# Kernel optimization log

Measured on AMD Instinct MI355X. Metric: run time of the kernel, lower is better.

The kernel has to match this reference:

```python
import jax, jax.numpy as jnp
import numpy as np

GRAY = 0.2989 + 0.5870 + 0.1140  # tf.image.rgb_to_grayscale weight sum (channels identical after grayscale_to_rgb)


def _resample(img, coords, axis):
    """Bilinear 1-D resample of `img` along `axis` at float `coords` (clamped)."""
    n = img.shape[axis]
    i0f = jnp.floor(coords)
    i0 = jnp.clip(i0f, 0, n - 1).astype(jnp.int32)
    i1 = jnp.clip(i0f + 1.0, 0, n - 1).astype(jnp.int32)
    f = coords - i0f
    a = jnp.take(img, i0, axis=axis)
    b = jnp.take(img, i1, axis=axis)
    shp = [1] * img.ndim
    shp[axis] = -1
    f = f.reshape(shp)
    return a * (1.0 - f) + b * f


def _aug_one(img, off_f, b, c, size, docrop, flp, k):
    S = img.shape[0]
    # ---- random crop (prob 0.5) + bilinear resize back to SxS (half-pixel centers) ----
    size_f = jnp.where(docrop, size.astype(jnp.float32), float(S))
    off = jnp.where(docrop, jnp.floor(off_f * (S - size_f + 1.0)), 0.0)  # [2] integer-valued offsets
    idx = (jnp.arange(S, dtype=jnp.float32) + 0.5) * (size_f / S) - 0.5
    img = _resample(img, idx + off[0], 0)
    img = _resample(img, idx + off[1], 1)
    # ---- random flip_left_right + rot90(k) ----
    img = jnp.where(flp, img[:, ::-1, :], img)
    rots = jnp.stack([img,
                      jnp.rot90(img, 1, (0, 1)),
                      jnp.rot90(img, 2, (0, 1)),
                      jnp.rot90(img, 3, (0, 1))])
    img = rots[k]
    # ---- per-channel brightness + contrast (gray->rgb->gray round trip == GRAY scale) ----
    x = img + b  # [S,S,C] + [C]
    m = jnp.mean(x, axis=(0, 1), keepdims=True)
    x = (x - m) * c + m
    return x * GRAY


def setup_inputs() -> dict:
    B, S, C = 64, 256, 5
    key = jax.random.key(0)
    ks = jax.random.split(key, 8)
    crops = jax.random.normal(ks[0], (B, S, S, C), dtype=jnp.float32)
    crop_size = jax.random.randint(ks[1], (B,), int(0.8 * S), S, dtype=jnp.int32)
    do_crop = jax.random.uniform(ks[2], (B,)) < 0.5
    off_frac = jax.random.uniform(ks[3], (B, 2), dtype=jnp.float32)
    flip = jax.random.uniform(ks[4], (B,)) < 0.5
    rot_k = jax.random.randint(ks[5], (B,), 0, 4, dtype=jnp.int32)
    bright = jax.random.uniform(ks[6], (B, C), minval=-0.1, maxval=0.1, dtype=jnp.float32)
    contrast = jax.random.uniform(ks[7], (B, C), minval=0.8, maxval=1.2, dtype=jnp.float32)
    return {"crops": crops, "off_frac": off_frac, "bright": bright, "contrast": contrast,
            "crop_size": crop_size, "do_crop": do_crop, "flip": flip, "rot_k": rot_k}


def reference(crops, off_frac, bright, contrast, crop_size, do_crop, flip, rot_k):
    return jax.vmap(_aug_one)(crops, off_frac, bright, contrast, crop_size, do_crop, flip, rot_k)
```

## Files before the change

### kernel.cpp

```cpp
#include <hip/hip_runtime.h>
#include <math.h>

#define SDIM 256
#define CH 5
#define ROWF (SDIM * CH)
#define NCHUNK 32
#define CHROWS 8
#define GRAYF 0.9999f

__global__ __launch_bounds__(256) void aug_sums_kernel(
    const float* __restrict__ crops,
    const float* __restrict__ off_frac,
    const int*   __restrict__ crop_size,
    const int*   __restrict__ do_crop,
    float* __restrict__ part)
{
    const int chunk = blockIdx.x;
    const int b     = blockIdx.y;
    const int tid   = threadIdx.x;

    __shared__ __align__(16) float wyl[SDIM];
    __shared__ __align__(16) float wxl[SDIM];
    __shared__ float psum[4][CH];

    const bool  docrop = do_crop[b] != 0;
    const float size_f = docrop ? (float)crop_size[b] : 256.0f;
    const float scale  = size_f * (1.0f / 256.0f);
    const float span   = 256.0f - size_f + 1.0f;
    const float off0   = docrop ? floorf(off_frac[2 * b + 0] * span) : 0.0f;
    const float off1   = docrop ? floorf(off_frac[2 * b + 1] * span) : 0.0f;

    wyl[tid] = 0.0f;
    wxl[tid] = 0.0f;
    __syncthreads();

    {
        const float cy = ((float)tid + 0.5f) * scale - 0.5f + off0;
        const float fl = floorf(cy);
        const float fy = cy - fl;
        const int r0 = min(max((int)fl, 0), 255);
        const int r1 = min(max((int)fl + 1, 0), 255);
        atomicAdd(&wyl[r0], 1.0f - fy);
        atomicAdd(&wyl[r1], fy);

        const float cx = ((float)tid + 0.5f) * scale - 0.5f + off1;
        const float fl2 = floorf(cx);
        const float fx  = cx - fl2;
        const int c0 = min(max((int)fl2, 0), 255);
        const int c1 = min(max((int)fl2 + 1, 0), 255);
        atomicAdd(&wxl[c0], 1.0f - fx);
        atomicAdd(&wxl[c1], fx);
    }
    __syncthreads();

    const float* srcbase = crops + ((size_t)b * SDIM + (size_t)chunk * CHROWS) * ROWF;
    const int rA = tid >> 6;
    const int rB = rA + 4;
    const int t  = tid & 63;

    const float4* pA = reinterpret_cast<const float4*>(srcbase + rA * ROWF + t * 20);
    const float4* pB = reinterpret_cast<const float4*>(srcbase + rB * ROWF + t * 20);
    const float4 a0 = pA[0], a1 = pA[1], a2 = pA[2], a3 = pA[3], a4 = pA[4];
    const float4 b0 = pB[0], b1 = pB[1], b2 = pB[2], b3 = pB[3], b4 = pB[4];

    const float wrA = wyl[chunk * CHROWS + rA];
    const float wrB = wyl[chunk * CHROWS + rB];
    const float4 wx = reinterpret_cast<const float4*>(wxl)[t];

    float acc[5] = {0.0f, 0.0f, 0.0f, 0.0f, 0.0f};
    {
        const float w0 = wx.x * wrA, w1 = wx.y * wrA, w2 = wx.z * wrA, w3 = wx.w * wrA;
        acc[0] += a0.x * w0; acc[1] += a0.y * w0; acc[2] += a0.z * w0; acc[3] += a0.w * w0;
        acc[4] += a1.x * w0; acc[0] += a1.y * w1; acc[1] += a1.z * w1; acc[2] += a1.w * w1;
        acc[3] += a2.x * w1; acc[4] += a2.y * w1; acc[0] += a2.z * w2; acc[1] += a2.w * w2;
        acc[2] += a3.x * w2; acc[3] += a3.y * w2; acc[4] += a3.z * w2; acc[0] += a3.w * w3;
        acc[1] += a4.x * w3; acc[2] += a4.y * w3; acc[3] += a4.z * w3; acc[4] += a4.w * w3;
    }
    {
        const float w0 = wx.x * wrB, w1 = wx.y * wrB, w2 = wx.z * wrB, w3 = wx.w * wrB;
        acc[0] += b0.x * w0; acc[1] += b0.y * w0; acc[2] += b0.z * w0; acc[3] += b0.w * w0;
        acc[4] += b1.x * w0; acc[0] += b1.y * w1; acc[1] += b1.z * w1; acc[2] += b1.w * w1;
        acc[3] += b2.x * w1; acc[4] += b2.y * w1; acc[0] += b2.z * w2; acc[1] += b2.w * w2;
        acc[2] += b3.x * w2; acc[3] += b3.y * w2; acc[4] += b3.z * w2; acc[0] += b3.w * w3;
        acc[1] += b4.x * w3; acc[2] += b4.y * w3; acc[3] += b4.z * w3; acc[4] += b4.w * w3;
    }

    const int lane = tid & 63;
    const int wv   = tid >> 6;
    #pragma unroll
    for (int ch = 0; ch < CH; ++ch) {
        float s = acc[ch];
        #pragma unroll
        for (int o = 32; o > 0; o >>= 1) s += __shfl_down(s, o, 64);
        if (lane == 0) psum[wv][ch] = s;
    }
    __syncthreads();
    if (tid == 0) {
        #pragma unroll
        for (int ch = 0; ch < CH; ++ch)
            part[((size_t)chunk * 64 + b) * CH + ch] =
                psum[0][ch] + psum[1][ch] + psum[2][ch] + psum[3][ch];
    }
}

__global__ __launch_bounds__(256) void aug_out_kernel(
    const float* __restrict__ crops,
    const float* __restrict__ off_frac,
    const int*   __restrict__ crop_size,
    const int*   __restrict__ do_crop,
    const int*   __restrict__ flip,
    const int*   __restrict__ rot_k,
    const float* __restrict__ part,
    const float* __restrict__ bright,
    const float* __restrict__ contrast,
    float* __restrict__ out)
{
    const int oi0  = blockIdx.x * 4;
    const int b    = blockIdx.y;
    const int tid  = threadIdx.x;
    const int rr   = tid >> 6;
    const int lane = tid & 63;

    __shared__ __align__(16) float smem[28 * 260];
    __shared__ float prm[2 * CH];

    const bool  docrop = do_crop[b] != 0;
    const float size_f = docrop ? (float)crop_size[b] : 256.0f;
    const float scale  = size_f * (1.0f / 256.0f);
    const float span   = 256.0f - size_f + 1.0f;
    const float off0   = docrop ? floorf(off_frac[2 * b + 0] * span) : 0.0f;
    const float off1   = docrop ? floorf(off_frac[2 * b + 1] * span) : 0.0f;
    const int   k      = rot_k[b] & 3;
    const bool  flp    = flip[b] != 0;

    if (tid < CH) {
        float s = 0.0f;
        #pragma unroll
        for (int p = 0; p < NCHUNK; ++p) s += part[((size_t)p * 64 + b) * CH + tid];
        const float m  = s * (1.0f / 65536.0f);
        const float co = contrast[b * CH + tid];
        const float br = bright[b * CH + tid];
        prm[tid]      = co * GRAYF;
        prm[CH + tid] = ((1.0f - co) * m + br) * GRAYF;
    }

    float vout[20];

    if ((k & 1) == 0) {
        const int y_min = (k == 0) ? oi0 : 255 - (oi0 + 3);
        const float cymin = ((float)y_min + 0.5f) * scale - 0.5f + off0;
        const int rbase = (int)floorf(cymin);
        const int nst   = docrop ? 5 : 4;

        const float4* src4 = reinterpret_cast<const float4*>(crops + (size_t)b * SDIM * ROWF);
        float4* dst4 = reinterpret_cast<float4*>(smem);
        for (int i = tid; i < nst * 320; i += 256) {
            const int w  = i / 320;
            const int f4 = i - w * 320;
            const int rc = min(max(rbase + w, 0), 255);
            dst4[i] = src4[rc * 320 + f4];
        }
        __syncthreads();

        const int oi = oi0 + rr;
        const int y  = (k == 0) ? oi : 255 - oi;

        if (!docrop) {
            const float* rb = smem + (y - rbase) * ROWF;
            #pragma unroll
            for (int p = 0; p < 4; ++p) {
                const int oj = lane + 64 * p;
                const int xf = (k == 0) ? oj : 255 - oj;
                const int x  = flp ? 255 - xf : xf;
                #pragma unroll
                for (int ch = 0; ch < CH; ++ch) vout[p * 5 + ch] = rb[x * CH + ch];
            }
        } else {
            const float cy  = ((float)y + 0.5f) * scale - 0.5f + off0;
            const float flr = floorf(cy);
            const float fy  = cy - flr;
            const float* rbA = smem + ((int)flr - rbase) * ROWF;
            const float* rbB = rbA + ROWF;
            #pragma unroll
            for (int p = 0; p < 4; ++p) {
                const int oj = lane + 64 * p;
                const int xf = (k == 0) ? oj : 255 - oj;
                const int x  = flp ? 255 - xf : xf;
                const float cx  = ((float)x + 0.5f) * scale - 0.5f + off1;
                const float fl2 = floorf(cx);
                const float fx  = cx - fl2;
                const int c0 = min(max((int)fl2, 0), 255);
                const int c1 = min(max((int)fl2 + 1, 0), 255);
                #pragma unroll
                for (int ch = 0; ch < CH; ++ch) {
                    const float aV = rbA[c0 * CH + ch] + fx * (rbA[c1 * CH + ch] - rbA[c0 * CH + ch]);
                    const float dV = rbB[c0 * CH + ch] + fx * (rbB[c1 * CH + ch] - rbB[c0 * CH + ch]);
                    vout[p * 5 + ch] = aV + fy * (dV - aV);
                }
            }
        }
    } else {
        const int xfA = (k == 1) ? 255 - oi0 : oi0;
        const int xfB = (k == 1) ? 255 - (oi0 + 3) : oi0 + 3;
        const int xA = flp ? 255 - xfA : xfA;
        const int xB = flp ? 255 - xfB : xfB;
        const int xmin = min(xA, xB);

        if (!docrop) {
            const int base4 = min((xmin * CH) & ~3, ROWF - 24);
            const float4* rp = reinterpret_cast<const float4*>(
                crops + ((size_t)b * SDIM + tid) * ROWF + base4);
            const float4 q0 = rp[0], q1 = rp[1], q2 = rp[2];
            const float4 q3 = rp[3], q4 = rp[4], q5 = rp[5];
            smem[ 0*260+tid]=q0.x; smem[ 1*260+tid]=q0.y; smem[ 2*260+tid]=q0.z; smem[ 3*260+tid]=q0.w;
            smem[ 4*260+tid]=q1.x; smem[ 5*260+tid]=q1.y; smem[ 6*260+tid]=q1.z; smem[ 7*260+tid]=q1.w;
            smem[ 8*260+tid]=q2.x; smem[ 9*260+tid]=q2.y; smem[10*260+tid]=q2.z; smem[11*260+tid]=q2.w;
            smem[12*260+tid]=q3.x; smem[13*260+tid]=q3.y; smem[14*260+tid]=q3.z; smem[15*260+tid]=q3.w;
            smem[16*260+tid]=q4.x; smem[17*260+tid]=q4.y; smem[18*260+tid]=q4.z; smem[19*260+tid]=q4.w;
            smem[20*260+tid]=q5.x; smem[21*260+tid]=q5.y; smem[22*260+tid]=q5.z; smem[23*260+tid]=q5.w;
            __syncthreads();

            const int oi = oi0 + rr;
            const int xf = (k == 1) ? 255 - oi : oi;
            const int x  = flp ? 255 - xf : xf;
            const int slotA = x * CH - base4;
            #pragma unroll
            for (int p = 0; p < 4; ++p) {
                const int oj = lane + 64 * p;
                const int y  = (k == 1) ? oj : 255 - oj;
                #pragma unroll
                for (int ch = 0; ch < CH; ++ch)
                    vout[p * 5 + ch] = smem[(slotA + ch) * 260 + y];
            }
        } else {
            const float cxmin = ((float)xmin + 0.5f) * scale - 0.5f + off1;
            const int cbase = (int)floorf(cxmin);
            const int base4 = (cbase * CH) & ~3;
            const bool fastp = (cbase >= 0) && (cbase + 4 <= 255) && (base4 >= 0) && (base4 + 28 <= ROWF);

            if (fastp) {
                const float4* rp = reinterpret_cast<const float4*>(
                    crops + ((size_t)b * SDIM + tid) * ROWF + base4);
                const float4 q0 = rp[0], q1 = rp[1], q2 = rp[2], q3 = rp[3];
                const float4 q4 = rp[4], q5 = rp[5], q6 = rp[6];
                smem[ 0*260+tid]=q0.x; smem[ 1*260+tid]=q0.y; smem[ 2*260+tid]=q0.z; smem[ 3*260+tid]=q0.w;
                smem[ 4*260+tid]=q1.x; smem[ 5*260+tid]=q1.y; smem[ 6*260+tid]=q1.z; smem[ 7*260+tid]=q1.w;
                smem[ 8*260+tid]=q2.x; smem[ 9*260+tid]=q2.y; smem[10*260+tid]=q2.z; smem[11*260+tid]=q2.w;
                smem[12*260+tid]=q3.x; smem[13*260+tid]=q3.y; smem[14*260+tid]=q3.z; smem[15*260+tid]=q3.w;
                smem[16*260+tid]=q4.x; smem[17*260+tid]=q4.y; smem[18*260+tid]=q4.z; smem[19*260+tid]=q4.w;
                smem[20*260+tid]=q5.x; smem[21*260+tid]=q5.y; smem[22*260+tid]=q5.z; smem[23*260+tid]=q5.w;
                smem[24*260+tid]=q6.x; smem[25*260+tid]=q6.y; smem[26*260+tid]=q6.z; smem[27*260+tid]=q6.w;
            } else {
                #pragma unroll
                for (int w = 0; w < 28; ++w) {
                    const int f2 = base4 + w + ROWF;
                    const int c2 = f2 / 5;
                    const int ch = f2 - c2 * 5;
                    const int cc = min(max(c2 - 256, 0), 255);
                    smem[w * 260 + tid] = crops[((size_t)b * SDIM + tid) * ROWF + cc * CH + ch];
                }
            }
            __syncthreads();

            const int oi = oi0 + rr;
            const int xf = (k == 1) ? 255 - oi : oi;
            const int x  = flp ? 255 - xf : xf;
            const float cx  = ((float)x + 0.5f) * scale - 0.5f + off1;
            const float fl2 = floorf(cx);
            const float fx  = cx - fl2;
            const int slotA = (int)fl2 * CH - base4;
            const int slotB = slotA + CH;

            #pragma unroll
            for (int p = 0; p < 4; ++p) {
                const int oj = lane + 64 * p;
                const int y  = (k == 1) ? oj : 255 - oj;
                const float cy  = ((float)y + 0.5f) * scale - 0.5f + off0;
                const float flr = floorf(cy);
                const float fy  = cy - flr;
                const int r0 = min(max((int)flr, 0), 255);
                const int r1 = min(max((int)flr + 1, 0), 255);
                #pragma unroll
                for (int ch = 0; ch < CH; ++ch) {
                    const float p00 = smem[(slotA + ch) * 260 + r0];
                    const float p01 = smem[(slotB + ch) * 260 + r0];
                    const float p10 = smem[(slotA + ch) * 260 + r1];
                    const float p11 = smem[(slotB + ch) * 260 + r1];
                    const float aV = p00 + fx * (p01 - p00);
                    const float dV = p10 + fx * (p11 - p10);
                    vout[p * 5 + ch] = aV + fy * (dV - aV);
                }
            }
        }
    }

    float aa[5], ab[5];
    #pragma unroll
    for (int ch = 0; ch < CH; ++ch) { aa[ch] = prm[ch]; ab[ch] = prm[CH + ch]; }
    #pragma unroll
    for (int p = 0; p < 4; ++p)
        #pragma unroll
        for (int ch = 0; ch < CH; ++ch)
            vout[p * 5 + ch] = vout[p * 5 + ch] * aa[ch] + ab[ch];

    __syncthreads();
    #pragma unroll
    for (int p = 0; p < 4; ++p) {
        const int oj = lane + 64 * p;
        #pragma unroll
        for (int ch = 0; ch < CH; ++ch)
            smem[rr * ROWF + oj * CH + ch] = vout[p * 5 + ch];
    }
    __syncthreads();

    const float4* ob4 = reinterpret_cast<const float4*>(smem);
    float4* dst = reinterpret_cast<float4*>(out + ((size_t)b * SDIM + oi0) * ROWF);
    #pragma unroll
    for (int q = 0; q < 5; ++q) dst[q * 256 + tid] = ob4[q * 256 + tid];
}

extern "C" void kernel_launch(void* const* d_in, const int* in_sizes, int n_in,
                              void* d_out, int out_size, void* d_ws, size_t ws_size,
                              hipStream_t stream) {
    const float* crops     = (const float*)d_in[0];
    const float* off_frac  = (const float*)d_in[1];
    const float* bright    = (const float*)d_in[2];
    const float* contrast  = (const float*)d_in[3];
    const int*   crop_size = (const int*)d_in[4];
    const int*   do_crop   = (const int*)d_in[5];
    const int*   flipb     = (const int*)d_in[6];
    const int*   rot_k     = (const int*)d_in[7];

    float* out  = (float*)d_out;
    float* part = (float*)d_ws;

    dim3 blk(256);
    aug_sums_kernel<<<dim3(NCHUNK, 64), blk, 0, stream>>>(crops, off_frac, crop_size, do_crop, part);
    aug_out_kernel<<<dim3(SDIM / 4, 64), blk, 0, stream>>>(crops, off_frac, crop_size, do_crop,
                                                           flipb, rot_k, part, bright, contrast, out);
}
```

Baseline: 184.3 us.

## Fuse mean-reduction and output kernels into one kernel with redundant per-block sums

Merges the partial-sum kernel and the output kernel into a single launch of 512 blocks, eight per image. Each block recomputes the full weighted channel mean for its image, then produces 32 output rows over 8 loop iterations. This removes the second launch and the workspace round trip for partial sums. In exchange, each image is read eight times for the reduction, and the grid is much smaller, which lowers parallelism and latency hiding.

```diff
diff --git a/kernel.cpp b/kernel.cpp
--- a/kernel.cpp
+++ b/kernel.cpp
@@ -4,24 +4,28 @@
 #define SDIM 256
 #define CH 5
 #define ROWF (SDIM * CH)
-#define NCHUNK 32
-#define CHROWS 8
 #define GRAYF 0.9999f
 
-__global__ __launch_bounds__(256) void aug_sums_kernel(
+__global__ __launch_bounds__(256) void aug_fused_kernel(
     const float* __restrict__ crops,
     const float* __restrict__ off_frac,
     const int*   __restrict__ crop_size,
     const int*   __restrict__ do_crop,
-    float* __restrict__ part)
+    const int*   __restrict__ flip,
+    const int*   __restrict__ rot_k,
+    const float* __restrict__ bright,
+    const float* __restrict__ contrast,
+    float* __restrict__ out)
 {
-    const int chunk = blockIdx.x;
-    const int b     = blockIdx.y;
-    const int tid   = threadIdx.x;
-
+    const int tid = threadIdx.x;
+    const int b   = blockIdx.x & 63;
+    const int pp  = blockIdx.x >> 6;
+
+    __shared__ __align__(16) float smem[28 * 260];
     __shared__ __align__(16) float wyl[SDIM];
     __shared__ __align__(16) float wxl[SDIM];
     __shared__ float psum[4][CH];
+    __shared__ float prm[2 * CH];
 
     const bool  docrop = do_crop[b] != 0;
     const float size_f = docrop ? (float)crop_size[b] : 256.0f;
@@ -29,11 +33,12 @@
     const float span   = 256.0f - size_f + 1.0f;
     const float off0   = docrop ? floorf(off_frac[2 * b + 0] * span) : 0.0f;
     const float off1   = docrop ? floorf(off_frac[2 * b + 1] * span) : 0.0f;
+    const int   k      = rot_k[b] & 3;
+    const bool  flp    = flip[b] != 0;
 
     wyl[tid] = 0.0f;
     wxl[tid] = 0.0f;
     __syncthreads();
-
     {
         const float cy = ((float)tid + 0.5f) * scale - 0.5f + off0;
         const float fl = floorf(cy);
@@ -53,36 +58,23 @@
     }
     __syncthreads();
 
-    const float* srcbase = crops + ((size_t)b * SDIM + (size_t)chunk * CHROWS) * ROWF;
-    const int rA = tid >> 6;
-    const int rB = rA + 4;
-    const int t  = tid & 63;
-
-    const float4* pA = reinterpret_cast<const float4*>(srcbase + rA * ROWF + t * 20);
-    const float4* pB = reinterpret_cast<const float4*>(srcbase + rB * ROWF + t * 20);
-    const float4 a0 = pA[0], a1 = pA[1], a2 = pA[2], a3 = pA[3], a4 = pA[4];
-    const float4 b0 = pB[0], b1 = pB[1], b2 = pB[2], b3 = pB[3], b4 = pB[4];
-
-    const float wrA = wyl[chunk * CHROWS + rA];
-    const float wrB = wyl[chunk * CHROWS + rB];
-    const float4 wx = reinterpret_cast<const float4*>(wxl)[t];
-
+    const float* srcbase = crops + (size_t)b * SDIM * ROWF;
     float acc[5] = {0.0f, 0.0f, 0.0f, 0.0f, 0.0f};
-    {
-        const float w0 = wx.x * wrA, w1 = wx.y * wrA, w2 = wx.z * wrA, w3 = wx.w * wrA;
-        acc[0] += a0.x * w0; acc[1] += a0.y * w0; acc[2] += a0.z * w0; acc[3] += a0.w * w0;
-        acc[4] += a1.x * w0; acc[0] += a1.y * w1; acc[1] += a1.z * w1; acc[2] += a1.w * w1;
-        acc[3] += a2.x * w1; acc[4] += a2.y * w1; acc[0] += a2.z * w2; acc[1] += a2.w * w2;
-        acc[2] += a3.x * w2; acc[3] += a3.y * w2; acc[4] += a3.z * w2; acc[0] += a3.w * w3;
-        acc[1] += a4.x * w3; acc[2] += a4.y * w3; acc[3] += a4.z * w3; acc[4] += a4.w * w3;
-    }
-    {
-        const float w0 = wx.x * wrB, w1 = wx.y * wrB, w2 = wx.z * wrB, w3 = wx.w * wrB;
-        acc[0] += b0.x * w0; acc[1] += b0.y * w0; acc[2] += b0.z * w0; acc[3] += b0.w * w0;
-        acc[4] += b1.x * w0; acc[0] += b1.y * w1; acc[1] += b1.z * w1; acc[2] += b1.w * w1;
-        acc[3] += b2.x * w1; acc[4] += b2.y * w1; acc[0] += b2.z * w2; acc[1] += b2.w * w2;
-        acc[2] += b3.x * w2; acc[3] += b3.y * w2; acc[4] += b3.z * w2; acc[0] += b3.w * w3;
-        acc[1] += b4.x * w3; acc[2] += b4.y * w3; acc[3] += b4.z * w3; acc[4] += b4.w * w3;
+    #pragma unroll 4
+    for (int it = 0; it < 64; ++it) {
+        const int m = it * 256 + tid;
+        const int r = m >> 6;
+        const int t = m & 63;
+        const float4* p4 = reinterpret_cast<const float4*>(srcbase + r * ROWF + t * 20);
+        const float4 q0 = p4[0], q1 = p4[1], q2 = p4[2], q3 = p4[3], q4 = p4[4];
+        const float wr = wyl[r];
+        const float4 wx = reinterpret_cast<const float4*>(wxl)[t];
+        const float w0 = wx.x * wr, w1 = wx.y * wr, w2 = wx.z * wr, w3 = wx.w * wr;
+        acc[0] += q0.x * w0; acc[1] += q0.y * w0; acc[2] += q0.z * w0; acc[3] += q0.w * w0;
+        acc[4] += q1.x * w0; acc[0] += q1.y * w1; acc[1] += q1.z * w1; acc[2] += q1.w * w1;
+        acc[3] += q2.x * w1; acc[4] += q2.y * w1; acc[0] += q2.z * w2; acc[1] += q2.w * w2;
+        acc[2] += q3.x * w2; acc[3] += q3.y * w2; acc[4] += q3.z * w2; acc[0] += q3.w * w3;
+        acc[1] += q4.x * w3; acc[2] += q4.y * w3; acc[3] += q4.z * w3; acc[4] += q4.w * w3;
     }
 
     const int lane = tid & 63;
@@ -95,48 +87,8 @@
         if (lane == 0) psum[wv][ch] = s;
     }
     __syncthreads();
-    if (tid == 0) {
-        #pragma unroll
-        for (int ch = 0; ch < CH; ++ch)
-            part[((size_t)chunk * 64 + b) * CH + ch] =
-                psum[0][ch] + psum[1][ch] + psum[2][ch] + psum[3][ch];
-    }
-}
-
-__global__ __launch_bounds__(256) void aug_out_kernel(
-    const float* __restrict__ crops,
-    const float* __restrict__ off_frac,
-    const int*   __restrict__ crop_size,
-    const int*   __restrict__ do_crop,
-    const int*   __restrict__ flip,
-    const int*   __restrict__ rot_k,
-    const float* __restrict__ part,
-    const float* __restrict__ bright,
-    const float* __restrict__ contrast,
-    float* __restrict__ out)
-{
-    const int oi0  = blockIdx.x * 4;
-    const int b    = blockIdx.y;
-    const int tid  = threadIdx.x;
-    const int rr   = tid >> 6;
-    const int lane = tid & 63;
-
-    __shared__ __align__(16) float smem[28 * 260];
-    __shared__ float prm[2 * CH];
-
-    const bool  docrop = do_crop[b] != 0;
-    const float size_f = docrop ? (float)crop_size[b] : 256.0f;
-    const float scale  = size_f * (1.0f / 256.0f);
-    const float span   = 256.0f - size_f + 1.0f;
-    const float off0   = docrop ? floorf(off_frac[2 * b + 0] * span) : 0.0f;
-    const float off1   = docrop ? floorf(off_frac[2 * b + 1] * span) : 0.0f;
-    const int   k      = rot_k[b] & 3;
-    const bool  flp    = flip[b] != 0;
-
     if (tid < CH) {
-        float s = 0.0f;
-        #pragma unroll
-        for (int p = 0; p < NCHUNK; ++p) s += part[((size_t)p * 64 + b) * CH + tid];
+        const float s  = psum[0][tid] + psum[1][tid] + psum[2][tid] + psum[3][tid];
         const float m  = s * (1.0f / 65536.0f);
         const float co = contrast[b * CH + tid];
         const float br = bright[b * CH + tid];
@@ -144,179 +96,186 @@
         prm[CH + tid] = ((1.0f - co) * m + br) * GRAYF;
     }
 
-    float vout[20];
-
-    if ((k & 1) == 0) {
-        const int y_min = (k == 0) ? oi0 : 255 - (oi0 + 3);
-        const float cymin = ((float)y_min + 0.5f) * scale - 0.5f + off0;
-        const int rbase = (int)floorf(cymin);
-        const int nst   = docrop ? 5 : 4;
-
-        const float4* src4 = reinterpret_cast<const float4*>(crops + (size_t)b * SDIM * ROWF);
-        float4* dst4 = reinterpret_cast<float4*>(smem);
-        for (int i = tid; i < nst * 320; i += 256) {
-            const int w  = i / 320;
-            const int f4 = i - w * 320;
-            const int rc = min(max(rbase + w, 0), 255);
-            dst4[i] = src4[rc * 320 + f4];
-        }
+    const int rr = tid >> 6;
+
+    for (int og = 0; og < 8; ++og) {
+        const int oi0 = pp * 32 + og * 4;
         __syncthreads();
 
-        const int oi = oi0 + rr;
-        const int y  = (k == 0) ? oi : 255 - oi;
-
-        if (!docrop) {
-            const float* rb = smem + (y - rbase) * ROWF;
-            #pragma unroll
-            for (int p = 0; p < 4; ++p) {
-                const int oj = lane + 64 * p;
-                const int xf = (k == 0) ? oj : 255 - oj;
-                const int x  = flp ? 255 - xf : xf;
-                #pragma unroll
-                for (int ch = 0; ch < CH; ++ch) vout[p * 5 + ch] = rb[x * CH + ch];
+        float vout[20];
+
+        if ((k & 1) == 0) {
+            const int y_min = (k == 0) ? oi0 : 255 - (oi0 + 3);
+            const float cymin = ((float)y_min + 0.5f) * scale - 0.5f + off0;
+            const int rbase = (int)floorf(cymin);
+            const int nst   = docrop ? 5 : 4;
+
+            const float4* src4 = reinterpret_cast<const float4*>(srcbase);
+            float4* dst4 = reinterpret_cast<float4*>(smem);
+            for (int i = tid; i < nst * 320; i += 256) {
+                const int w  = i / 320;
+                const int f4 = i - w * 320;
+                const int rc = min(max(rbase + w, 0), 255);
+                dst4[i] = src4[rc * 320 + f4];
+            }
+            __syncthreads();
+
+            const int oi = oi0 + rr;
+            const int y  = (k == 0) ? oi : 255 - oi;
+
+            if (!docrop) {
+                const float* rb = smem + (y - rbase) * ROWF;
+                #pragma unroll
+                for (int p = 0; p < 4; ++p) {
+                    const int oj = lane + 64 * p;
+                    const int xf = (k == 0) ? oj : 255 - oj;
+                    const int x  = flp ? 255 - xf : xf;
+                    #pragma unroll
+                    for (int ch = 0; ch < CH; ++ch) vout[p * 5 + ch] = rb[x * CH + ch];
+                }
+            } else {
+                const float cy  = ((float)y + 0.5f) * scale - 0.5f + off0;
+                const float flr = floorf(cy);
+                const float fy  = cy - flr;
+                const float* rbA = smem + ((int)flr - rbase) * ROWF;
+                const float* rbB = rbA + ROWF;
+                #pragma unroll
+                for (int p = 0; p < 4; ++p) {
+                    const int oj = lane + 64 * p;
+                    const int xf = (k == 0) ? oj : 255 - oj;
+                    const int x  = flp ? 255 - xf : xf;
+                    const float cx  = ((float)x + 0.5f) * scale - 0.5f + off1;
+                    const float fl2 = floorf(cx);
+                    const float fx  = cx - fl2;
+                    const int c0 = min(max((int)fl2, 0), 255);
+                    const int c1 = min(max((int)fl2 + 1, 0), 255);
+                    #pragma unroll
+                    for (int ch = 0; ch < CH; ++ch) {
+                        const float aV = rbA[c0 * CH + ch] + fx * (rbA[c1 * CH + ch] - rbA[c0 * CH + ch]);
+                        const float dV = rbB[c0 * CH + ch] + fx * (rbB[c1 * CH + ch] - rbB[c0 * CH + ch]);
+                        vout[p * 5 + ch] = aV + fy * (dV - aV);
+                    }
+                }
             }
         } else {
-            const float cy  = ((float)y + 0.5f) * scale - 0.5f + off0;
-            const float flr = floorf(cy);
-            const float fy  = cy - flr;
-            const float* rbA = smem + ((int)flr - rbase) * ROWF;
-            const float* rbB = rbA + ROWF;
-            #pragma unroll
-            for (int p = 0; p < 4; ++p) {
-                const int oj = lane + 64 * p;
-                const int xf = (k == 0) ? oj : 255 - oj;
-                const int x  = flp ? 255 - xf : xf;
-                const float cx  = ((float)x + 0.5f) * scale - 0.5f + off1;
-                const float fl2 = floorf(cx);
-                const float fx  = cx - fl2;
-                const int c0 = min(max((int)fl2, 0), 255);
-                const int c1 = min(max((int)fl2 + 1, 0), 255);
-                #pragma unroll
-                for (int ch = 0; ch < CH; ++ch) {
-                    const float aV = rbA[c0 * CH + ch] + fx * (rbA[c1 * CH + ch] - rbA[c0 * CH + ch]);
-                    const float dV = rbB[c0 * CH + ch] + fx * (rbB[c1 * CH + ch] - rbB[c0 * CH + ch]);
-                    vout[p * 5 + ch] = aV + fy * (dV - aV);
-                }
-            }
-        }
-    } else {
-        const int xfA = (k == 1) ? 255 - oi0 : oi0;
-        const int xfB = (k == 1) ? 255 - (oi0 + 3) : oi0 + 3;
-        const int xA = flp ? 255 - xfA : xfA;
-        const int xB = flp ? 255 - xfB : xfB;
-        const int xmin = min(xA, xB);
-
-        if (!docrop) {
-            const int base4 = min((xmin * CH) & ~3, ROWF - 24);
-            const float4* rp = reinterpret_cast<const float4*>(
-                crops + ((size_t)b * SDIM + tid) * ROWF + base4);
-            const float4 q0 = rp[0], q1 = rp[1], q2 = rp[2];
-            const float4 q3 = rp[3], q4 = rp[4], q5 = rp[5];
-            smem[ 0*260+tid]=q0.x; smem[ 1*260+tid]=q0.y; smem[ 2*260+tid]=q0.z; smem[ 3*260+tid]=q0.w;
-            smem[ 4*260+tid]=q1.x; smem[ 5*260+tid]=q1.y; smem[ 6*260+tid]=q1.z; smem[ 7*260+tid]=q1.w;
-            smem[ 8*260+tid]=q2.x; smem[ 9*260+tid]=q2.y; smem[10*260+tid]=q2.z; smem[11*260+tid]=q2.w;
-            smem[12*260+tid]=q3.x; smem[13*260+tid]=q3.y; smem[14*260+tid]=q3.z; smem[15*260+tid]=q3.w;
-            smem[16*260+tid]=q4.x; smem[17*260+tid]=q4.y; smem[18*260+tid]=q4.z; smem[19*260+tid]=q4.w;
-            smem[20*260+tid]=q5.x; smem[21*260+tid]=q5.y; smem[22*260+tid]=q5.z; smem[23*260+tid]=q5.w;
-            __syncthreads();
-
-            const int oi = oi0 + rr;
-            const int xf = (k == 1) ? 255 - oi : oi;
-            const int x  = flp ? 255 - xf : xf;
-            const int slotA = x * CH - base4;
-            #pragma unroll
-            for (int p = 0; p < 4; ++p) {
-                const int oj = lane + 64 * p;
-                const int y  = (k == 1) ? oj : 255 - oj;
-                #pragma unroll
-                for (int ch = 0; ch < CH; ++ch)
-                    vout[p * 5 + ch] = smem[(slotA + ch) * 260 + y];
-            }
-        } else {
-            const float cxmin = ((float)xmin + 0.5f) * scale - 0.5f + off1;
-            const int cbase = (int)floorf(cxmin);
-            const int base4 = (cbase * CH) & ~3;
-            const bool fastp = (cbase >= 0) && (cbase + 4 <= 255) && (base4 >= 0) && (base4 + 28 <= ROWF);
-
-            if (fastp) {
+            const int xfA = (k == 1) ? 255 - oi0 : oi0;
+            const int xfB = (k == 1) ? 255 - (oi0 + 3) : oi0 + 3;
+            const int xA = flp ? 255 - xfA : xfA;
+            const int xB = flp ? 255 - xfB : xfB;
+            const int xmin = min(xA, xB);
+
+            if (!docrop) {
+                const int base4 = min((xmin * CH) & ~3, ROWF - 24);
                 const float4* rp = reinterpret_cast<const float4*>(
-                    crops + ((size_t)b * SDIM + tid) * ROWF + base4);
-                const float4 q0 = rp[0], q1 = rp[1], q2 = rp[2], q3 = rp[3];
-                const float4 q4 = rp[4], q5 = rp[5], q6 = rp[6];
+                    srcbase + (size_t)tid * ROWF + base4);
+                const float4 q0 = rp[0], q1 = rp[1], q2 = rp[2];
+                const float4 q3 = rp[3], q4 = rp[4], q5 = rp[5];
                 smem[ 0*260+tid]=q0.x; smem[ 1*260+tid]=q0.y; smem[ 2*260+tid]=q0.z; smem[ 3*260+tid]=q0.w;
                 smem[ 4*260+tid]=q1.x; smem[ 5*260+tid]=q1.y; smem[ 6*260+tid]=q1.z; smem[ 7*260+tid]=q1.w;
                 smem[ 8*260+tid]=q2.x; smem[ 9*260+tid]=q2.y; smem[10*260+tid]=q2.z; smem[11*260+tid]=q2.w;
                 smem[12*260+tid]=q3.x; smem[13*260+tid]=q3.y; smem[14*260+tid]=q3.z; smem[15*260+tid]=q3.w;
                 smem[16*260+tid]=q4.x; smem[17*260+tid]=q4.y; smem[18*260+tid]=q4.z; smem[19*260+tid]=q4.w;
                 smem[20*260+tid]=q5.x; smem[21*260+tid]=q5.y; smem[22*260+tid]=q5.z; smem[23*260+tid]=q5.w;
-                smem[24*260+tid]=q6.x; smem[25*260+tid]=q6.y; smem[26*260+tid]=q6.z; smem[27*260+tid]=q6.w;
+                __syncthreads();
+
+                const int oi = oi0 + rr;
+                const int xf = (k == 1) ? 255 - oi : oi;
+                const int x  = flp ? 255 - xf : xf;
+                const int slotA = x * CH - base4;
+                #pragma unroll
+                for (int p = 0; p < 4; ++p) {
+                    const int oj = lane + 64 * p;
+                    const int y  = (k == 1) ? oj : 255 - oj;
+                    #pragma unroll
+                    for (int ch = 0; ch < CH; ++ch)
+                        vout[p * 5 + ch] = smem[(slotA + ch) * 260 + y];
+                }
             } else {
-                #pragma unroll
-                for (int w = 0; w < 28; ++w) {
-                    const int f2 = base4 + w + ROWF;
-                    const int c2 = f2 / 5;
-                    const int ch = f2 - c2 * 5;
-                    const int cc = min(max(c2 - 256, 0), 255);
-                    smem[w * 260 + tid] = crops[((size_t)b * SDIM + tid) * ROWF + cc * CH + ch];
-                }
-            }
-            __syncthreads();
-
-            const int oi = oi0 + rr;
-            const int xf = (k == 1) ? 255 - oi : oi;
-            const int x  = flp ? 255 - xf : xf;
-            const float cx  = ((float)x + 0.5f) * scale - 0.5f + off1;
-            const float fl2 = floorf(cx);
-            const float fx  = cx - fl2;
-            const int slotA = (int)fl2 * CH - base4;
-            const int slotB = slotA + CH;
-
-            #pragma unroll
-            for (int p = 0; p < 4; ++p) {
-                const int oj = lane + 64 * p;
-                const int y  = (k == 1) ? oj : 255 - oj;
-                const float cy  = ((float)y + 0.5f) * scale - 0.5f + off0;
-                const float flr = floorf(cy);
-                const float fy  = cy - flr;
-                const int r0 = min(max((int)flr, 0), 255);
-                const int r1 = min(max((int)flr + 1, 0), 255);
-                #pragma unroll
-                for (int ch = 0; ch < CH; ++ch) {
-                    const float p00 = smem[(slotA + ch) * 260 + r0];
-                    const float p01 = smem[(slotB + ch) * 260 + r0];
-                    const float p10 = smem[(slotA + ch) * 260 + r1];
-                    const float p11 = smem[(slotB + ch) * 260 + r1];
-                    const float aV = p00 + fx * (p01 - p00);
-                    const float dV = p10 + fx * (p11 - p10);
-                    vout[p * 5 + ch] = aV + fy * (dV - aV);
+                const float cxmin = ((float)xmin + 0.5f) * scale - 0.5f + off1;
+                const int cbase = (int)floorf(cxmin);
+                const int base4 = (cbase * CH) & ~3;
+                const bool fastp = (cbase >= 0) && (cbase + 4 <= 255) && (base4 >= 0) && (base4 + 28 <= ROWF);
+
+                if (fastp) {
+                    const float4* rp = reinterpret_cast<const float4*>(
+                        srcbase + (size_t)tid * ROWF + base4);
+                    const float4 q0 = rp[0], q1 = rp[1], q2 = rp[2], q3 = rp[3];
+                    const float4 q4 = rp[4], q5 = rp[5], q6 = rp[6];
+                    smem[ 0*260+tid]=q0.x; smem[ 1*260+tid]=q0.y; smem[ 2*260+tid]=q0.z; smem[ 3*260+tid]=q0.w;
+                    smem[ 4*260+tid]=q1.x; smem[ 5*260+tid]=q1.y; smem[ 6*260+tid]=q1.z; smem[ 7*260+tid]=q1.w;
+                    smem[ 8*260+tid]=q2.x; smem[ 9*260+tid]=q2.y; smem[10*260+tid]=q2.z; smem[11*260+tid]=q2.w;
+                    smem[12*260+tid]=q3.x; smem[13*260+tid]=q3.y; smem[14*260+tid]=q3.z; smem[15*260+tid]=q3.w;
+                    smem[16*260+tid]=q4.x; smem[17*260+tid]=q4.y; smem[18*260+tid]=q4.z; smem[19*260+tid]=q4.w;
+                    smem[20*260+tid]=q5.x; smem[21*260+tid]=q5.y; smem[22*260+tid]=q5.z; smem[23*260+tid]=q5.w;
+                    smem[24*260+tid]=q6.x; smem[25*260+tid]=q6.y; smem[26*260+tid]=q6.z; smem[27*260+tid]=q6.w;
+                } else {
+                    #pragma unroll
+                    for (int w = 0; w < 28; ++w) {
+                        const int f2 = base4 + w + ROWF;
+                        const int c2 = f2 / 5;
+                        const int ch = f2 - c2 * 5;
+                        const int cc = min(max(c2 - 256, 0), 255);
+                        smem[w * 260 + tid] = srcbase[(size_t)tid * ROWF + cc * CH + ch];
+                    }
+                }
+                __syncthreads();
+
+                const int oi = oi0 + rr;
+                const int xf = (k == 1) ? 255 - oi : oi;
+                const int x  = flp ? 255 - xf : xf;
+                const float cx  = ((float)x + 0.5f) * scale - 0.5f + off1;
+                const float fl2 = floorf(cx);
+                const float fx  = cx - fl2;
+                const int slotA = (int)fl2 * CH - base4;
+                const int slotB = slotA + CH;
+
+                #pragma unroll
+                for (int p = 0; p < 4; ++p) {
+                    const int oj = lane + 64 * p;
+                    const int y  = (k == 1) ? oj : 255 - oj;
+                    const float cy  = ((float)y + 0.5f) * scale - 0.5f + off0;
+                    const float flr = floorf(cy);
+                    const float fy  = cy - flr;
+                    const int r0 = min(max((int)flr, 0), 255);
+                    const int r1 = min(max((int)flr + 1, 0), 255);
+                    #pragma unroll
+                    for (int ch = 0; ch < CH; ++ch) {
+                        const float p00 = smem[(slotA + ch) * 260 + r0];
+                        const float p01 = smem[(slotB + ch) * 260 + r0];
+                        const float p10 = smem[(slotA + ch) * 260 + r1];
+                        const float p11 = smem[(slotB + ch) * 260 + r1];
+                        const float aV = p00 + fx * (p01 - p00);
+                        const float dV = p10 + fx * (p11 - p10);
+                        vout[p * 5 + ch] = aV + fy * (dV - aV);
+                    }
                 }
             }
         }
-    }
-
-    float aa[5], ab[5];
-    #pragma unroll
-    for (int ch = 0; ch < CH; ++ch) { aa[ch] = prm[ch]; ab[ch] = prm[CH + ch]; }
-    #pragma unroll
-    for (int p = 0; p < 4; ++p)
-        #pragma unroll
-        for (int ch = 0; ch < CH; ++ch)
-            vout[p * 5 + ch] = vout[p * 5 + ch] * aa[ch] + ab[ch];
-
-    __syncthreads();
-    #pragma unroll
-    for (int p = 0; p < 4; ++p) {
-        const int oj = lane + 64 * p;
-        #pragma unroll
-        for (int ch = 0; ch < CH; ++ch)
-            smem[rr * ROWF + oj * CH + ch] = vout[p * 5 + ch];
-    }
-    __syncthreads();
-
-    const float4* ob4 = reinterpret_cast<const float4*>(smem);
-    float4* dst = reinterpret_cast<float4*>(out + ((size_t)b * SDIM + oi0) * ROWF);
-    #pragma unroll
-    for (int q = 0; q < 5; ++q) dst[q * 256 + tid] = ob4[q * 256 + tid];
+
+        float aa[5], ab[5];
+        #pragma unroll
+        for (int ch = 0; ch < CH; ++ch) { aa[ch] = prm[ch]; ab[ch] = prm[CH + ch]; }
+        #pragma unroll
+        for (int p = 0; p < 4; ++p)
+            #pragma unroll
+            for (int ch = 0; ch < CH; ++ch)
+                vout[p * 5 + ch] = vout[p * 5 + ch] * aa[ch] + ab[ch];
+
+        __syncthreads();
+        #pragma unroll
+        for (int p = 0; p < 4; ++p) {
+            const int oj = lane + 64 * p;
+            #pragma unroll
+            for (int ch = 0; ch < CH; ++ch)
+                smem[rr * ROWF + oj * CH + ch] = vout[p * 5 + ch];
+        }
+        __syncthreads();
+
+        const float4* ob4 = reinterpret_cast<const float4*>(smem);
+        float4* dst = reinterpret_cast<float4*>(out + ((size_t)b * SDIM + oi0) * ROWF);
+        #pragma unroll
+        for (int q = 0; q < 5; ++q) dst[q * 256 + tid] = ob4[q * 256 + tid];
+    }
 }
 
 extern "C" void kernel_launch(void* const* d_in, const int* in_sizes, int n_in,
@@ -331,11 +290,8 @@
     const int*   flipb     = (const int*)d_in[6];
     const int*   rot_k     = (const int*)d_in[7];
 
-    float* out  = (float*)d_out;
-    float* part = (float*)d_ws;
-
-    dim3 blk(256);
-    aug_sums_kernel<<<dim3(NCHUNK, 64), blk, 0, stream>>>(crops, off_frac, crop_size, do_crop, part);
-    aug_out_kernel<<<dim3(SDIM / 4, 64), blk, 0, stream>>>(crops, off_frac, crop_size, do_crop,
-                                                           flipb, rot_k, part, bright, contrast, out);
+    float* out = (float*)d_out;
+
+    aug_fused_kernel<<<dim3(512), dim3(256), 0, stream>>>(
+        crops, off_frac, crop_size, do_crop, flipb, rot_k, bright, contrast, out);
 }
```

Measured after the change: 228.1 us. 23.8% more time.
